# Optimization experiments

Hardware: AMD Instinct MI355X
Metric: run time of the kernel (lower is better)

Reference implementation:

```python
import jax, jax.numpy as jnp
import numpy as np

N = 100000
E = 3200000
F_IN = 128
HID = 128
NC = 10
G = 512  # number of graphs in batch


def setup_inputs() -> dict:
    key = jax.random.key(0)
    ks = jax.random.split(key, 9)
    x = jax.random.normal(ks[0], (N, F_IN), dtype=jnp.float32)
    edge_index = jax.random.randint(ks[1], (2, E), 0, N, dtype=jnp.int64)
    batch = jnp.sort(jax.random.randint(ks[2], (N,), 0, G, dtype=jnp.int64))
    s = 1.0 / np.sqrt(F_IN)
    W1 = jax.random.uniform(ks[3], (F_IN, HID), jnp.float32, -s, s)
    b1 = jnp.zeros((HID,), jnp.float32)
    sh = 1.0 / np.sqrt(HID)
    W2 = jax.random.uniform(ks[4], (HID, HID), jnp.float32, -sh, sh)
    b2 = jnp.zeros((HID,), jnp.float32)
    Wc = jax.random.uniform(ks[5], (HID, NC), jnp.float32, -sh, sh)
    bc = jax.random.uniform(ks[6], (NC,), jnp.float32, -sh, sh)
    return {"x": x, "edge_index": edge_index, "batch": batch,
            "W1": W1, "b1": b1, "W2": W2, "b2": b2, "Wc": Wc, "bc": bc}


def _gcn_conv(x, src, dst, norm, W, b):
    # linear transform first (PyG GCNConv), then normalized scatter-add
    h = x @ W                              # [N, H]
    msg = h[src] * norm[:, None]           # gather + scale, [E+N, H]
    out = jax.ops.segment_sum(msg, dst, num_segments=N)
    return out + b


def reference(x, edge_index, batch, W1, b1, W2, b2, Wc, bc):
    # add self-loops (PyG gcn_norm default)
    loop = jnp.arange(N, dtype=edge_index.dtype)
    src = jnp.concatenate([edge_index[0], loop])
    dst = jnp.concatenate([edge_index[1], loop])
    deg = jax.ops.segment_sum(jnp.ones_like(dst, dtype=x.dtype), dst, num_segments=N)
    dis = jnp.where(deg > 0, jax.lax.rsqrt(deg), 0.0)  # deg^{-1/2}
    norm = dis[src] * dis[dst]

    h = jax.nn.relu(_gcn_conv(x, src, dst, norm, W1, b1))
    # dropout is identity in eval mode
    h = jax.nn.relu(_gcn_conv(h, src, dst, norm, W2, b2))

    # global mean pool over graph ids
    sums = jax.ops.segment_sum(h, batch, num_segments=G)
    cnts = jax.ops.segment_sum(jnp.ones((N,), h.dtype), batch, num_segments=G)
    pooled = sums / jnp.maximum(cnts, 1.0)[:, None]   # [G, HID]

    logits = pooled @ Wc + bc                          # [G, NC]
    return logits, pooled
```

## Files before the change

### kernel.cpp

```cpp
#include <hip/hip_runtime.h>
#include <hip/hip_bf16.h>

typedef short bf16x8 __attribute__((ext_vector_type(8)));
typedef float f32x4 __attribute__((ext_vector_type(4)));
typedef unsigned int u32x4 __attribute__((ext_vector_type(4)));

__device__ __forceinline__ unsigned short f2bf(float f) {
    unsigned int u = __float_as_uint(f);
    unsigned int r = u + 0x7fffu + ((u >> 16) & 1u);
    return (unsigned short)(r >> 16);
}
__device__ __forceinline__ float bf2f(unsigned short b) {
    return __uint_as_float(((unsigned int)b) << 16);
}
__device__ __forceinline__ unsigned int packbf2(float lo, float hi) {
    return ((unsigned int)f2bf(hi) << 16) | (unsigned int)f2bf(lo);
}

__global__ __launch_bounds__(256) void hist_k(const int* __restrict__ dst, int* __restrict__ hist,
                                              int e, int nbuk, int nblk, int eb) {
    __shared__ int lh[512];
    int blk = blockIdx.x, t = threadIdx.x;
    for (int j = t; j < nbuk; j += 256) lh[j] = 0;
    __syncthreads();
    int e0 = blk * eb, e1 = min(e, e0 + eb);
    for (int i = e0 + t; i < e1; i += 256) atomicAdd(&lh[dst[i] >> 8], 1);
    __syncthreads();
    for (int j = t; j < nbuk; j += 256) hist[(size_t)j * nblk + blk] = lh[j];
}

__global__ __launch_bounds__(256) void scanA_k(int* __restrict__ hist, int* __restrict__ btot, int nbuk, int nblk) {
    int w = (blockIdx.x * 256 + threadIdx.x) >> 6;
    int lane = threadIdx.x & 63;
    if (w >= nbuk) return;
    size_t base = (size_t)w * nblk;
    int run = 0;
    for (int c = 0; c < nblk; c += 64) {
        int i = c + lane;
        int v = (i < nblk) ? hist[base + i] : 0;
        int orig = v;
        for (int d = 1; d < 64; d <<= 1) { int u = __shfl_up(v, d); if (lane >= d) v += u; }
        if (i < nblk) hist[base + i] = run + v - orig;
        run += __shfl(v, 63);
    }
    if (lane == 0) btot[w] = run;
}

__global__ __launch_bounds__(512) void scanB_k(const int* __restrict__ btot, int* __restrict__ bbase, int nbuk) {
    __shared__ int s[512];
    int t = threadIdx.x;
    int v = (t < nbuk) ? btot[t] : 0;
    s[t] = v;
    __syncthreads();
    for (int st = 1; st < 512; st <<= 1) {
        int add = (t >= st) ? s[t - st] : 0;
        __syncthreads();
        s[t] += add;
        __syncthreads();
    }
    if (t < nbuk) bbase[t] = s[t] - v;
    if (t == nbuk - 1) bbase[nbuk] = s[t];
}

__global__ __launch_bounds__(256) void scatter_k(const int* __restrict__ src, const int* __restrict__ dst,
                                                 const int* __restrict__ hist, const int* __restrict__ bbase,
                                                 unsigned int* __restrict__ coarse, int e, int nbuk, int nblk, int eb) {
    __shared__ int cur[512];
    int blk = blockIdx.x, t = threadIdx.x;
    for (int j = t; j < nbuk; j += 256) cur[j] = bbase[j] + hist[(size_t)j * nblk + blk];
    __syncthreads();
    int e0 = blk * eb, e1 = min(e, e0 + eb);
    for (int i = e0 + t; i < e1; i += 256) {
        int s = src[i], d = dst[i];
        int bk = d >> 8;
        int p = atomicAdd(&cur[bk], 1);
        coarse[p] = ((unsigned int)(d & 255) << 24) | (unsigned int)s;
    }
}

__global__ __launch_bounds__(256) void bucket_k(const unsigned int* __restrict__ coarse, const int* __restrict__ bbase,
                                                float* __restrict__ dis, int* __restrict__ row_ptr, int* __restrict__ col,
                                                int n, int nbuk, int e) {
    __shared__ int h[256];
    __shared__ int s[256];
    __shared__ int cur[256];
    int b = blockIdx.x, t = threadIdx.x;
    int e0 = bbase[b], e1 = bbase[b + 1];
    h[t] = 0;
    __syncthreads();
    for (int i = e0 + t; i < e1; i += 256) atomicAdd(&h[coarse[i] >> 24], 1);
    __syncthreads();
    int v = h[t];
    s[t] = v;
    __syncthreads();
    for (int st = 1; st < 256; st <<= 1) {
        int add = (t >= st) ? s[t - st] : 0;
        __syncthreads();
        s[t] += add;
        __syncthreads();
    }
    int excl = s[t] - v;
    int node = b * 256 + t;
    if (node < n) {
        row_ptr[node] = e0 + excl;
        dis[node] = rsqrtf((float)v + 1.0f);
    }
    cur[t] = e0 + excl;
    __syncthreads();
    for (int i = e0 + t; i < e1; i += 256) {
        unsigned int pk = coarse[i];
        int p = atomicAdd(&cur[pk >> 24], 1);
        col[p] = (int)(pk & 0x00FFFFFFu);
    }
    if (b == nbuk - 1 && t == 0) row_ptr[n] = e;
}

template <bool INF32>
__global__ __launch_bounds__(256) void gemm_mfma_k(const void* __restrict__ Av, const float* __restrict__ W,
                                                   const float* __restrict__ dis, unsigned short* __restrict__ C,
                                                   int nrows) {
    __shared__ unsigned short WT[128 * 136];
    int t = threadIdx.x;
    for (int i = t; i < 16384; i += 256) {
        int k = i >> 7, nn = i & 127;
        WT[nn * 136 + k] = f2bf(W[i]);
    }
    __syncthreads();
    int wave = t >> 6, lane = t & 63;
    int lm = lane & 15, lg = lane >> 4;
    for (int m0 = blockIdx.x * 64; m0 < nrows; m0 += gridDim.x * 64) {
        int R = m0 + wave * 16;
        int arow = R + lm;
        if (arow >= nrows) arow = nrows - 1;
        f32x4 acc[8];
#pragma unroll
        for (int q = 0; q < 8; q++) acc[q] = (f32x4){0.f, 0.f, 0.f, 0.f};
#pragma unroll
        for (int kk = 0; kk < 4; kk++) {
            bf16x8 af;
            if constexpr (INF32) {
                const float4* ap = (const float4*)((const float*)Av + (size_t)arow * 128 + kk * 32 + lg * 8);
                float4 a0 = ap[0], a1 = ap[1];
                u32x4 au;
                au[0] = packbf2(a0.x, a0.y); au[1] = packbf2(a0.z, a0.w);
                au[2] = packbf2(a1.x, a1.y); au[3] = packbf2(a1.z, a1.w);
                af = __builtin_bit_cast(bf16x8, au);
            } else {
                const u32x4* ap = (const u32x4*)((const unsigned short*)Av + (size_t)arow * 128);
                af = __builtin_bit_cast(bf16x8, ap[kk * 4 + lg]);
            }
#pragma unroll
            for (int q = 0; q < 8; q++) {
                const u32x4* bp = (const u32x4*)(WT + (q * 16 + lm) * 136 + kk * 32 + lg * 8);
                bf16x8 bfr = __builtin_bit_cast(bf16x8, *bp);
                acc[q] = __builtin_amdgcn_mfma_f32_16x16x32_bf16(af, bfr, acc[q], 0, 0, 0);
            }
        }
        float dsc[4];
#pragma unroll
        for (int i2 = 0; i2 < 4; i2++) {
            int r = R + lg * 4 + i2;
            dsc[i2] = (r < nrows) ? dis[r] : 0.f;
        }
#pragma unroll
        for (int i2 = 0; i2 < 4; i2++) {
            int r = R + lg * 4 + i2;
            if (r < nrows) {
                unsigned short* cp = C + (size_t)r * 128 + lm;
#pragma unroll
                for (int q = 0; q < 8; q++) cp[q * 16] = f2bf(acc[q][i2] * dsc[i2]);
            }
        }
    }
}

__global__ __launch_bounds__(256) void agg_k(const unsigned short* __restrict__ h, unsigned short* __restrict__ out,
                                             const int* __restrict__ row_ptr, const int* __restrict__ col,
                                             const float* __restrict__ dis, const float* __restrict__ bias, int n) {
    int wid  = (blockIdx.x * 256 + threadIdx.x) >> 6;
    int lane = threadIdx.x & 63;
    if (wid >= n) return;
    int g = lane >> 4;
    int s = lane & 15;
    const char* hb = (const char*)h;
    unsigned int soff = (unsigned int)(s << 4);
    float acc0 = 0.f, acc1 = 0.f, acc2 = 0.f, acc3 = 0.f;
    float acc4 = 0.f, acc5 = 0.f, acc6 = 0.f, acc7 = 0.f;
#define ACCUM(v)                                                                              \
    acc0 += __uint_as_float((v)[0] << 16); acc1 += __uint_as_float((v)[0] & 0xffff0000u);     \
    acc2 += __uint_as_float((v)[1] << 16); acc3 += __uint_as_float((v)[1] & 0xffff0000u);     \
    acc4 += __uint_as_float((v)[2] << 16); acc5 += __uint_as_float((v)[2] & 0xffff0000u);     \
    acc6 += __uint_as_float((v)[3] << 16); acc7 += __uint_as_float((v)[3] & 0xffff0000u);
    if (g == 0) {
        u32x4 v = *(const u32x4*)(hb + (((unsigned int)wid << 8) + soff));
        ACCUM(v)
    }
    int e = row_ptr[wid] + g, e1 = row_ptr[wid + 1];
    for (; e + 12 < e1; e += 16) {
        int c0 = col[e], c1 = col[e + 4], c2 = col[e + 8], c3 = col[e + 12];
        u32x4 v0 = *(const u32x4*)(hb + (((unsigned int)c0 << 8) + soff));
        u32x4 v1 = *(const u32x4*)(hb + (((unsigned int)c1 << 8) + soff));
        u32x4 v2 = *(const u32x4*)(hb + (((unsigned int)c2 << 8) + soff));
        u32x4 v3 = *(const u32x4*)(hb + (((unsigned int)c3 << 8) + soff));
        ACCUM(v0)
        ACCUM(v1)
        ACCUM(v2)
        ACCUM(v3)
    }
    for (; e < e1; e += 4) {
        u32x4 v = *(const u32x4*)(hb + (((unsigned int)col[e] << 8) + soff));
        ACCUM(v)
    }
#undef ACCUM
#define RED(a) a += __shfl_xor(a, 16); a += __shfl_xor(a, 32);
    RED(acc0) RED(acc1) RED(acc2) RED(acc3) RED(acc4) RED(acc5) RED(acc6) RED(acc7)
#undef RED
    if (g == 0) {
        float d = dis[wid];
        const float4* bp = (const float4*)bias;
        float4 ba = bp[2 * s], bb = bp[2 * s + 1];
        u32x4 r;
        r[0] = packbf2(fmaxf(ba.x + d * acc0, 0.f), fmaxf(ba.y + d * acc1, 0.f));
        r[1] = packbf2(fmaxf(ba.z + d * acc2, 0.f), fmaxf(ba.w + d * acc3, 0.f));
        r[2] = packbf2(fmaxf(bb.x + d * acc4, 0.f), fmaxf(bb.y + d * acc5, 0.f));
        r[3] = packbf2(fmaxf(bb.z + d * acc6, 0.f), fmaxf(bb.w + d * acc7, 0.f));
        *(u32x4*)((char*)out + (((unsigned int)wid << 8) + soff)) = r;
    }
}

__global__ __launch_bounds__(128) void pool_logits_k(const unsigned short* __restrict__ h, const int* __restrict__ batch,
                                                     const float* __restrict__ Wc, const float* __restrict__ bc,
                                                     float* __restrict__ logits, float* __restrict__ pooled,
                                                     int n, int nc) {
    __shared__ float pl[128];
    int g = blockIdx.x;
    int j = threadIdx.x;
    int lo = 0, hi = n;
    while (lo < hi) { int mid = (lo + hi) >> 1; if (batch[mid] < g) lo = mid + 1; else hi = mid; }
    int start = lo;
    hi = n;
    while (lo < hi) { int mid = (lo + hi) >> 1; if (batch[mid] < g + 1) lo = mid + 1; else hi = mid; }
    int end = lo;
    float acc = 0.f;
    for (int r = start; r < end; r++) acc += bf2f(h[(size_t)r * 128 + j]);
    float pv = acc / fmaxf((float)(end - start), 1.0f);
    pooled[(size_t)g * 128 + j] = pv;
    pl[j] = pv;
    __syncthreads();
    if (j < nc) {
        float a = bc[j];
#pragma unroll 8
        for (int k = 0; k < 128; k++) a += pl[k] * Wc[k * nc + j];
        logits[(size_t)g * nc + j] = a;
    }
}

extern "C" void kernel_launch(void* const* d_in, const int* in_sizes, int n_in,
                              void* d_out, int out_size, void* d_ws, size_t ws_size,
                              hipStream_t stream) {
    const float* x     = (const float*)d_in[0];
    const int*   ei    = (const int*)d_in[1];
    const int*   batch = (const int*)d_in[2];
    const float* W1    = (const float*)d_in[3];
    const float* b1    = (const float*)d_in[4];
    const float* W2    = (const float*)d_in[5];
    const float* b2    = (const float*)d_in[6];
    const float* Wc    = (const float*)d_in[7];
    const float* bc    = (const float*)d_in[8];
    float* out = (float*)d_out;

    const int N = in_sizes[0] / 128;
    const int E = in_sizes[1] / 2;
    const int NC = 10;
    const int G = out_size / (NC + 128);

    const int* src = ei;
    const int* dst = ei + E;

    const int EB   = 16384;
    const int NBLK = (E + EB - 1) / EB;
    const int NBUK = (N + 255) / 256;

    char* wbase = (char*)d_ws;
    size_t off = 0;
    auto alloc = [&](size_t bytes) -> void* {
        void* p = wbase + off;
        off = (off + bytes + 255) & ~(size_t)255;
        return p;
    };
    float* dis     = (float*)alloc((size_t)N * 4);
    int*   row_ptr = (int*)alloc((size_t)(N + 1) * 4);
    int*   hist    = (int*)alloc((size_t)NBUK * NBLK * 4);
    int*   btot    = (int*)alloc((size_t)NBUK * 4);
    int*   bbase   = (int*)alloc((size_t)(NBUK + 1) * 4);
    unsigned int* coarse = (unsigned int*)alloc((size_t)E * 4);
    int*   col     = (int*)alloc((size_t)E * 4);
    unsigned short* bufT = (unsigned short*)alloc((size_t)N * 128 * 2);
    unsigned short* bufH = (unsigned short*)alloc((size_t)N * 128 * 2);

    hist_k<<<NBLK, 256, 0, stream>>>(dst, hist, E, NBUK, NBLK, EB);
    scanA_k<<<(NBUK * 64 + 255) / 256, 256, 0, stream>>>(hist, btot, NBUK, NBLK);
    scanB_k<<<1, 512, 0, stream>>>(btot, bbase, NBUK);
    scatter_k<<<NBLK, 256, 0, stream>>>(src, dst, hist, bbase, coarse, E, NBUK, NBLK, EB);
    bucket_k<<<NBUK, 256, 0, stream>>>(coarse, bbase, dis, row_ptr, col, N, NBUK, E);

    gemm_mfma_k<true><<<512, 256, 0, stream>>>(x, W1, dis, bufT, N);
    agg_k<<<(N + 3) / 4, 256, 0, stream>>>(bufT, bufH, row_ptr, col, dis, b1, N);
    gemm_mfma_k<false><<<512, 256, 0, stream>>>(bufH, W2, dis, bufT, N);
    agg_k<<<(N + 3) / 4, 256, 0, stream>>>(bufT, bufH, row_ptr, col, dis, b2, N);

    float* pooled = out + (size_t)G * NC;
    pool_logits_k<<<G, 128, 0, stream>>>(bufH, batch, Wc, bc, out, pooled, N, NC);
}
```

Baseline: 401.4 us.

## Presort edges by source bucket before destination bucketing for gather locality

Adds a first LSD-style radix pass that buckets edges by the high bits of the source index, then a stable second pass by destination bucket. Within each CSR row the neighbor columns come out roughly ordered by source, which is meant to improve cache locality of the feature gathers in the aggregation kernels. In exchange it adds a full extra histogram, scan and scatter pass over 3.2M edges, plus two extra E-sized buffers.

```diff
diff --git a/kernel.cpp b/kernel.cpp
--- a/kernel.cpp
+++ b/kernel.cpp
@@ -17,14 +17,14 @@
     return ((unsigned int)f2bf(hi) << 16) | (unsigned int)f2bf(lo);
 }
 
-__global__ __launch_bounds__(256) void hist_k(const int* __restrict__ dst, int* __restrict__ hist,
-                                              int e, int nbuk, int nblk, int eb) {
+__global__ __launch_bounds__(256) void histk_k(const int* __restrict__ key, int* __restrict__ hist,
+                                               int e, int nbuk, int nblk, int eb) {
     __shared__ int lh[512];
     int blk = blockIdx.x, t = threadIdx.x;
     for (int j = t; j < nbuk; j += 256) lh[j] = 0;
     __syncthreads();
     int e0 = blk * eb, e1 = min(e, e0 + eb);
-    for (int i = e0 + t; i < e1; i += 256) atomicAdd(&lh[dst[i] >> 8], 1);
+    for (int i = e0 + t; i < e1; i += 256) atomicAdd(&lh[key[i] >> 8], 1);
     __syncthreads();
     for (int j = t; j < nbuk; j += 256) hist[(size_t)j * nblk + blk] = lh[j];
 }
@@ -62,9 +62,10 @@
     if (t == nbuk - 1) bbase[nbuk] = s[t];
 }
 
-__global__ __launch_bounds__(256) void scatter_k(const int* __restrict__ src, const int* __restrict__ dst,
-                                                 const int* __restrict__ hist, const int* __restrict__ bbase,
-                                                 unsigned int* __restrict__ coarse, int e, int nbuk, int nblk, int eb) {
+__global__ __launch_bounds__(256) void scatter1_k(const int* __restrict__ src, const int* __restrict__ dst,
+                                                  const int* __restrict__ hist, const int* __restrict__ bbase,
+                                                  int* __restrict__ es_s, int* __restrict__ es_d,
+                                                  int e, int nbuk, int nblk, int eb) {
     __shared__ int cur[512];
     int blk = blockIdx.x, t = threadIdx.x;
     for (int j = t; j < nbuk; j += 256) cur[j] = bbase[j] + hist[(size_t)j * nblk + blk];
@@ -72,8 +73,24 @@
     int e0 = blk * eb, e1 = min(e, e0 + eb);
     for (int i = e0 + t; i < e1; i += 256) {
         int s = src[i], d = dst[i];
-        int bk = d >> 8;
-        int p = atomicAdd(&cur[bk], 1);
+        int p = atomicAdd(&cur[s >> 8], 1);
+        es_s[p] = s;
+        es_d[p] = d;
+    }
+}
+
+__global__ __launch_bounds__(256) void scatter2_k(const int* __restrict__ es_s, const int* __restrict__ es_d,
+                                                  const int* __restrict__ hist, const int* __restrict__ bbase,
+                                                  unsigned int* __restrict__ coarse,
+                                                  int e, int nbuk, int nblk, int eb) {
+    __shared__ int cur[512];
+    int blk = blockIdx.x, t = threadIdx.x;
+    for (int j = t; j < nbuk; j += 256) cur[j] = bbase[j] + hist[(size_t)j * nblk + blk];
+    __syncthreads();
+    int e0 = blk * eb, e1 = min(e, e0 + eb);
+    for (int i = e0 + t; i < e1; i += 256) {
+        int s = es_s[i], d = es_d[i];
+        int p = atomicAdd(&cur[d >> 8], 1);
         coarse[p] = ((unsigned int)(d & 255) << 24) | (unsigned int)s;
     }
 }
@@ -290,19 +307,27 @@
     };
     float* dis     = (float*)alloc((size_t)N * 4);
     int*   row_ptr = (int*)alloc((size_t)(N + 1) * 4);
-    int*   hist    = (int*)alloc((size_t)NBUK * NBLK * 4);
+    int*   hist1   = (int*)alloc((size_t)NBUK * NBLK * 4);
+    int*   hist2   = (int*)alloc((size_t)NBUK * NBLK * 4);
     int*   btot    = (int*)alloc((size_t)NBUK * 4);
-    int*   bbase   = (int*)alloc((size_t)(NBUK + 1) * 4);
+    int*   bbase1  = (int*)alloc((size_t)(NBUK + 1) * 4);
+    int*   bbase2  = (int*)alloc((size_t)(NBUK + 1) * 4);
+    int*   es_s    = (int*)alloc((size_t)E * 4);
+    int*   es_d    = (int*)alloc((size_t)E * 4);
     unsigned int* coarse = (unsigned int*)alloc((size_t)E * 4);
     int*   col     = (int*)alloc((size_t)E * 4);
     unsigned short* bufT = (unsigned short*)alloc((size_t)N * 128 * 2);
     unsigned short* bufH = (unsigned short*)alloc((size_t)N * 128 * 2);
 
-    hist_k<<<NBLK, 256, 0, stream>>>(dst, hist, E, NBUK, NBLK, EB);
-    scanA_k<<<(NBUK * 64 + 255) / 256, 256, 0, stream>>>(hist, btot, NBUK, NBLK);
-    scanB_k<<<1, 512, 0, stream>>>(btot, bbase, NBUK);
-    scatter_k<<<NBLK, 256, 0, stream>>>(src, dst, hist, bbase, coarse, E, NBUK, NBLK, EB);
-    bucket_k<<<NBUK, 256, 0, stream>>>(coarse, bbase, dis, row_ptr, col, N, NBUK, E);
+    histk_k<<<NBLK, 256, 0, stream>>>(src, hist1, E, NBUK, NBLK, EB);
+    scanA_k<<<(NBUK * 64 + 255) / 256, 256, 0, stream>>>(hist1, btot, NBUK, NBLK);
+    scanB_k<<<1, 512, 0, stream>>>(btot, bbase1, NBUK);
+    scatter1_k<<<NBLK, 256, 0, stream>>>(src, dst, hist1, bbase1, es_s, es_d, E, NBUK, NBLK, EB);
+    histk_k<<<NBLK, 256, 0, stream>>>(es_d, hist2, E, NBUK, NBLK, EB);
+    scanA_k<<<(NBUK * 64 + 255) / 256, 256, 0, stream>>>(hist2, btot, NBUK, NBLK);
+    scanB_k<<<1, 512, 0, stream>>>(btot, bbase2, NBUK);
+    scatter2_k<<<NBLK, 256, 0, stream>>>(es_s, es_d, hist2, bbase2, coarse, E, NBUK, NBLK, EB);
+    bucket_k<<<NBUK, 256, 0, stream>>>(coarse, bbase2, dis, row_ptr, col, N, NBUK, E);
 
     gemm_mfma_k<true><<<512, 256, 0, stream>>>(x, W1, dis, bufT, N);
     agg_k<<<(N + 3) / 4, 256, 0, stream>>>(bufT, bufH, row_ptr, col, dis, b1, N);
```

Result: slower. 471.0 us (+17.3%).

## Partition CSR by source-node tiles and aggregate many nodes per wave tile-by-tile

Applied to the files above, without the earlier changes.

The CSR build now buckets edges by source tile (2^14 nodes) as well as destination bucket, which yields T per-tile row pointer arrays. A separate kernel derives degrees and the dis normalisation from those pointers. The aggregation kernel has each wave handle 25 consecutive nodes and walk the source tiles in order, so gathered feature rows come from a bounded working set that should stay resident in L2/MALL. The cost is more histogram buckets, a larger scan, and a serial per-wave loop over many nodes with 4-byte-per-lane loads, which cuts memory-level parallelism and can cause load imbalance.

```diff
diff --git a/kernel.cpp b/kernel.cpp
--- a/kernel.cpp
+++ b/kernel.cpp
@@ -16,17 +16,25 @@
 __device__ __forceinline__ unsigned int packbf2(float lo, float hi) {
     return ((unsigned int)f2bf(hi) << 16) | (unsigned int)f2bf(lo);
 }
-
-__global__ __launch_bounds__(256) void hist_k(const int* __restrict__ dst, int* __restrict__ hist,
-                                              int e, int nbuk, int nblk, int eb) {
-    __shared__ int lh[512];
+__device__ __forceinline__ float bflo(unsigned int v) { return __uint_as_float(v << 16); }
+__device__ __forceinline__ float bfhi(unsigned int v) { return __uint_as_float(v & 0xffff0000u); }
+
+#define TSHIFT 14
+
+__global__ __launch_bounds__(256) void hist2_k(const int* __restrict__ src, const int* __restrict__ dst,
+                                               int* __restrict__ hist, int e, int B, int nbukd,
+                                               int nblk, int eb) {
+    __shared__ int lh[4096];
     int blk = blockIdx.x, t = threadIdx.x;
-    for (int j = t; j < nbuk; j += 256) lh[j] = 0;
+    for (int j = t; j < 4096; j += 256) lh[j] = 0;
     __syncthreads();
     int e0 = blk * eb, e1 = min(e, e0 + eb);
-    for (int i = e0 + t; i < e1; i += 256) atomicAdd(&lh[dst[i] >> 8], 1);
-    __syncthreads();
-    for (int j = t; j < nbuk; j += 256) hist[(size_t)j * nblk + blk] = lh[j];
+    for (int i = e0 + t; i < e1; i += 256) {
+        int k = (src[i] >> TSHIFT) * nbukd + (dst[i] >> 8);
+        atomicAdd(&lh[k], 1);
+    }
+    __syncthreads();
+    for (int j = t; j < B; j += 256) hist[(size_t)j * nblk + blk] = lh[j];
 }
 
 __global__ __launch_bounds__(256) void scanA_k(int* __restrict__ hist, int* __restrict__ btot, int nbuk, int nblk) {
@@ -46,41 +54,51 @@
     if (lane == 0) btot[w] = run;
 }
 
-__global__ __launch_bounds__(512) void scanB_k(const int* __restrict__ btot, int* __restrict__ bbase, int nbuk) {
+__global__ __launch_bounds__(512) void scanBbig_k(const int* __restrict__ btot, int* __restrict__ bbase, int B) {
     __shared__ int s[512];
+    __shared__ int carry;
     int t = threadIdx.x;
-    int v = (t < nbuk) ? btot[t] : 0;
-    s[t] = v;
-    __syncthreads();
-    for (int st = 1; st < 512; st <<= 1) {
-        int add = (t >= st) ? s[t - st] : 0;
-        __syncthreads();
-        s[t] += add;
-        __syncthreads();
-    }
-    if (t < nbuk) bbase[t] = s[t] - v;
-    if (t == nbuk - 1) bbase[nbuk] = s[t];
-}
-
-__global__ __launch_bounds__(256) void scatter_k(const int* __restrict__ src, const int* __restrict__ dst,
-                                                 const int* __restrict__ hist, const int* __restrict__ bbase,
-                                                 unsigned int* __restrict__ coarse, int e, int nbuk, int nblk, int eb) {
-    __shared__ int cur[512];
+    if (t == 0) carry = 0;
+    __syncthreads();
+    for (int c0 = 0; c0 < B; c0 += 512) {
+        int idx = c0 + t;
+        int v = (idx < B) ? btot[idx] : 0;
+        s[t] = v;
+        __syncthreads();
+        for (int st = 1; st < 512; st <<= 1) {
+            int add = (t >= st) ? s[t - st] : 0;
+            __syncthreads();
+            s[t] += add;
+            __syncthreads();
+        }
+        if (idx < B) bbase[idx] = carry + s[t] - v;
+        __syncthreads();
+        if (t == 511) carry += s[511];
+        __syncthreads();
+    }
+    if (t == 0) bbase[B] = carry;
+}
+
+__global__ __launch_bounds__(256) void scatter2_k(const int* __restrict__ src, const int* __restrict__ dst,
+                                                  const int* __restrict__ hist, const int* __restrict__ bbase,
+                                                  unsigned int* __restrict__ coarse, int e, int B, int nbukd,
+                                                  int nblk, int eb) {
+    __shared__ int cur[4096];
     int blk = blockIdx.x, t = threadIdx.x;
-    for (int j = t; j < nbuk; j += 256) cur[j] = bbase[j] + hist[(size_t)j * nblk + blk];
+    for (int j = t; j < B; j += 256) cur[j] = bbase[j] + hist[(size_t)j * nblk + blk];
     __syncthreads();
     int e0 = blk * eb, e1 = min(e, e0 + eb);
     for (int i = e0 + t; i < e1; i += 256) {
         int s = src[i], d = dst[i];
-        int bk = d >> 8;
-        int p = atomicAdd(&cur[bk], 1);
+        int k = (s >> TSHIFT) * nbukd + (d >> 8);
+        int p = atomicAdd(&cur[k], 1);
         coarse[p] = ((unsigned int)(d & 255) << 24) | (unsigned int)s;
     }
 }
 
-__global__ __launch_bounds__(256) void bucket_k(const unsigned int* __restrict__ coarse, const int* __restrict__ bbase,
-                                                float* __restrict__ dis, int* __restrict__ row_ptr, int* __restrict__ col,
-                                                int n, int nbuk, int e) {
+__global__ __launch_bounds__(256) void bucket2_k(const unsigned int* __restrict__ coarse, const int* __restrict__ bbase,
+                                                 int* __restrict__ rpt, int* __restrict__ col,
+                                                 int n, int nbukd, int B, int T) {
     __shared__ int h[256];
     __shared__ int s[256];
     __shared__ int cur[256];
@@ -100,11 +118,10 @@
         __syncthreads();
     }
     int excl = s[t] - v;
-    int node = b * 256 + t;
-    if (node < n) {
-        row_ptr[node] = e0 + excl;
-        dis[node] = rsqrtf((float)v + 1.0f);
-    }
+    int tt = b / nbukd;
+    int db = b - tt * nbukd;
+    int gnode = db * 256 + t;
+    if (gnode < n) rpt[(size_t)tt * n + gnode] = e0 + excl;
     cur[t] = e0 + excl;
     __syncthreads();
     for (int i = e0 + t; i < e1; i += 256) {
@@ -112,7 +129,15 @@
         int p = atomicAdd(&cur[pk >> 24], 1);
         col[p] = (int)(pk & 0x00FFFFFFu);
     }
-    if (b == nbuk - 1 && t == 0) row_ptr[n] = e;
+    if (b == B - 1 && t == 0) rpt[(size_t)T * n] = e1;
+}
+
+__global__ __launch_bounds__(256) void degdis_k(const int* __restrict__ rpt, float* __restrict__ dis, int n, int T) {
+    int i = blockIdx.x * 256 + threadIdx.x;
+    if (i >= n) return;
+    int d = 0;
+    for (int t = 0; t < T; t++) d += rpt[(size_t)t * n + i + 1] - rpt[(size_t)t * n + i];
+    dis[i] = rsqrtf((float)d + 1.0f);
 }
 
 template <bool INF32>
@@ -174,57 +199,60 @@
     }
 }
 
-__global__ __launch_bounds__(256) void agg_k(const unsigned short* __restrict__ h, unsigned short* __restrict__ out,
-                                             const int* __restrict__ row_ptr, const int* __restrict__ col,
-                                             const float* __restrict__ dis, const float* __restrict__ bias, int n) {
+template <int KN>
+__global__ __launch_bounds__(256, 4) void agg_tiled_k(const unsigned short* __restrict__ h,
+                                                      unsigned short* __restrict__ out,
+                                                      const int* __restrict__ rpt, const int* __restrict__ col,
+                                                      const float* __restrict__ dis, const float* __restrict__ bias,
+                                                      int n, int T) {
     int wid  = (blockIdx.x * 256 + threadIdx.x) >> 6;
     int lane = threadIdx.x & 63;
-    if (wid >= n) return;
-    int g = lane >> 4;
-    int s = lane & 15;
-    const char* hb = (const char*)h;
-    unsigned int soff = (unsigned int)(s << 4);
-    float acc0 = 0.f, acc1 = 0.f, acc2 = 0.f, acc3 = 0.f;
-    float acc4 = 0.f, acc5 = 0.f, acc6 = 0.f, acc7 = 0.f;
-#define ACCUM(v)                                                                              \
-    acc0 += __uint_as_float((v)[0] << 16); acc1 += __uint_as_float((v)[0] & 0xffff0000u);     \
-    acc2 += __uint_as_float((v)[1] << 16); acc3 += __uint_as_float((v)[1] & 0xffff0000u);     \
-    acc4 += __uint_as_float((v)[2] << 16); acc5 += __uint_as_float((v)[2] & 0xffff0000u);     \
-    acc6 += __uint_as_float((v)[3] << 16); acc7 += __uint_as_float((v)[3] & 0xffff0000u);
-    if (g == 0) {
-        u32x4 v = *(const u32x4*)(hb + (((unsigned int)wid << 8) + soff));
-        ACCUM(v)
-    }
-    int e = row_ptr[wid] + g, e1 = row_ptr[wid + 1];
-    for (; e + 12 < e1; e += 16) {
-        int c0 = col[e], c1 = col[e + 4], c2 = col[e + 8], c3 = col[e + 12];
-        u32x4 v0 = *(const u32x4*)(hb + (((unsigned int)c0 << 8) + soff));
-        u32x4 v1 = *(const u32x4*)(hb + (((unsigned int)c1 << 8) + soff));
-        u32x4 v2 = *(const u32x4*)(hb + (((unsigned int)c2 << 8) + soff));
-        u32x4 v3 = *(const u32x4*)(hb + (((unsigned int)c3 << 8) + soff));
-        ACCUM(v0)
-        ACCUM(v1)
-        ACCUM(v2)
-        ACCUM(v3)
-    }
-    for (; e < e1; e += 4) {
-        u32x4 v = *(const u32x4*)(hb + (((unsigned int)col[e] << 8) + soff));
-        ACCUM(v)
-    }
-#undef ACCUM
-#define RED(a) a += __shfl_xor(a, 16); a += __shfl_xor(a, 32);
-    RED(acc0) RED(acc1) RED(acc2) RED(acc3) RED(acc4) RED(acc5) RED(acc6) RED(acc7)
-#undef RED
-    if (g == 0) {
-        float d = dis[wid];
-        const float4* bp = (const float4*)bias;
-        float4 ba = bp[2 * s], bb = bp[2 * s + 1];
-        u32x4 r;
-        r[0] = packbf2(fmaxf(ba.x + d * acc0, 0.f), fmaxf(ba.y + d * acc1, 0.f));
-        r[1] = packbf2(fmaxf(ba.z + d * acc2, 0.f), fmaxf(ba.w + d * acc3, 0.f));
-        r[2] = packbf2(fmaxf(bb.x + d * acc4, 0.f), fmaxf(bb.y + d * acc5, 0.f));
-        r[3] = packbf2(fmaxf(bb.z + d * acc6, 0.f), fmaxf(bb.w + d * acc7, 0.f));
-        *(u32x4*)((char*)out + (((unsigned int)wid << 8) + soff)) = r;
+    int node0 = wid * KN;
+    if (node0 >= n) return;
+    const unsigned int* hp = (const unsigned int*)h;
+    float accx[KN], accy[KN];
+#pragma unroll
+    for (int i = 0; i < KN; i++) { accx[i] = 0.f; accy[i] = 0.f; }
+#pragma unroll
+    for (int i = 0; i < KN; i++) {
+        int nd = node0 + i;
+        if (nd < n) {
+            unsigned int v = hp[((size_t)nd << 6) + lane];
+            accx[i] += bflo(v);
+            accy[i] += bfhi(v);
+        }
+    }
+    for (int t = 0; t < T; t++) {
+        const int* rp = rpt + (size_t)t * n;
+#pragma unroll
+        for (int i = 0; i < KN; i++) {
+            int nd = node0 + i;
+            if (nd < n) {
+                int e = rp[nd], e1 = rp[nd + 1];
+                for (; e + 2 <= e1; e += 2) {
+                    int c0 = col[e], c1 = col[e + 1];
+                    unsigned int v0 = hp[((size_t)c0 << 6) + lane];
+                    unsigned int v1 = hp[((size_t)c1 << 6) + lane];
+                    accx[i] += bflo(v0) + bflo(v1);
+                    accy[i] += bfhi(v0) + bfhi(v1);
+                }
+                if (e < e1) {
+                    unsigned int v = hp[((size_t)col[e] << 6) + lane];
+                    accx[i] += bflo(v);
+                    accy[i] += bfhi(v);
+                }
+            }
+        }
+    }
+    float2 b = ((const float2*)bias)[lane];
+#pragma unroll
+    for (int i = 0; i < KN; i++) {
+        int nd = node0 + i;
+        if (nd < n) {
+            float d = dis[nd];
+            ((unsigned int*)out)[((size_t)nd << 6) + lane] =
+                packbf2(fmaxf(b.x + d * accx[i], 0.f), fmaxf(b.y + d * accy[i], 0.f));
+        }
     }
 }
 
@@ -277,9 +305,11 @@
     const int* src = ei;
     const int* dst = ei + E;
 
-    const int EB   = 16384;
-    const int NBLK = (E + EB - 1) / EB;
-    const int NBUK = (N + 255) / 256;
+    const int EB    = 16384;
+    const int NBLK  = (E + EB - 1) / EB;
+    const int NBUKD = (N + 255) / 256;
+    const int T     = (N + (1 << TSHIFT) - 1) >> TSHIFT;
+    const int B     = T * NBUKD;
 
     char* wbase = (char*)d_ws;
     size_t off = 0;
@@ -288,26 +318,29 @@
         off = (off + bytes + 255) & ~(size_t)255;
         return p;
     };
-    float* dis     = (float*)alloc((size_t)N * 4);
-    int*   row_ptr = (int*)alloc((size_t)(N + 1) * 4);
-    int*   hist    = (int*)alloc((size_t)NBUK * NBLK * 4);
-    int*   btot    = (int*)alloc((size_t)NBUK * 4);
-    int*   bbase   = (int*)alloc((size_t)(NBUK + 1) * 4);
+    float* dis   = (float*)alloc((size_t)N * 4);
+    int*   rpt   = (int*)alloc(((size_t)T * N + 1) * 4);
+    int*   hist  = (int*)alloc((size_t)B * NBLK * 4);
+    int*   btot  = (int*)alloc((size_t)B * 4);
+    int*   bbase = (int*)alloc((size_t)(B + 1) * 4);
     unsigned int* coarse = (unsigned int*)alloc((size_t)E * 4);
-    int*   col     = (int*)alloc((size_t)E * 4);
+    int*   col   = (int*)alloc((size_t)E * 4);
     unsigned short* bufT = (unsigned short*)alloc((size_t)N * 128 * 2);
     unsigned short* bufH = (unsigned short*)alloc((size_t)N * 128 * 2);
 
-    hist_k<<<NBLK, 256, 0, stream>>>(dst, hist, E, NBUK, NBLK, EB);
-    scanA_k<<<(NBUK * 64 + 255) / 256, 256, 0, stream>>>(hist, btot, NBUK, NBLK);
-    scanB_k<<<1, 512, 0, stream>>>(btot, bbase, NBUK);
-    scatter_k<<<NBLK, 256, 0, stream>>>(src, dst, hist, bbase, coarse, E, NBUK, NBLK, EB);
-    bucket_k<<<NBUK, 256, 0, stream>>>(coarse, bbase, dis, row_ptr, col, N, NBUK, E);
-
+    hist2_k<<<NBLK, 256, 0, stream>>>(src, dst, hist, E, B, NBUKD, NBLK, EB);
+    scanA_k<<<(B * 64 + 255) / 256, 256, 0, stream>>>(hist, btot, B, NBLK);
+    scanBbig_k<<<1, 512, 0, stream>>>(btot, bbase, B);
+    scatter2_k<<<NBLK, 256, 0, stream>>>(src, dst, hist, bbase, coarse, E, B, NBUKD, NBLK, EB);
+    bucket2_k<<<B, 256, 0, stream>>>(coarse, bbase, rpt, col, N, NBUKD, B, T);
+    degdis_k<<<(N + 255) / 256, 256, 0, stream>>>(rpt, dis, N, T);
+
+    constexpr int KN = 25;
+    const int aggBlocks = (N + KN * 4 - 1) / (KN * 4);
     gemm_mfma_k<true><<<512, 256, 0, stream>>>(x, W1, dis, bufT, N);
-    agg_k<<<(N + 3) / 4, 256, 0, stream>>>(bufT, bufH, row_ptr, col, dis, b1, N);
+    agg_tiled_k<KN><<<aggBlocks, 256, 0, stream>>>(bufT, bufH, rpt, col, dis, b1, N, T);
     gemm_mfma_k<false><<<512, 256, 0, stream>>>(bufH, W2, dis, bufT, N);
-    agg_k<<<(N + 3) / 4, 256, 0, stream>>>(bufT, bufH, row_ptr, col, dis, b2, N);
+    agg_tiled_k<KN><<<aggBlocks, 256, 0, stream>>>(bufT, bufH, rpt, col, dis, b2, N, T);
 
     float* pooled = out + (size_t)G * NC;
     pool_logits_k<<<G, 128, 0, stream>>>(bufH, batch, Wc, bc, out, pooled, N, NC);
```

After: 825.7 us. +105.7%, slower.
